# Optimization experiments

Hardware: AMD Instinct MI355X
Metric: run time of the kernel (lower is better)

## Reference

```python
import jax, jax.numpy as jnp
import numpy as np

NUM_HEADS = 4


def lin_interp(f, out_len):
    """Matches torch F.interpolate(mode='linear', align_corners=False) on (B, L_in, D)."""
    L_in = f.shape[1]
    if L_in == out_len:
        return f
    scale = L_in / out_len
    src = (jnp.arange(out_len, dtype=f.dtype) + 0.5) * scale - 0.5
    src = jnp.clip(src, 0.0, L_in - 1)
    i0 = jnp.floor(src).astype(jnp.int32)
    i1 = jnp.minimum(i0 + 1, L_in - 1)
    w = (src - i0.astype(f.dtype))[None, :, None]
    return f[:, i0, :] * (1.0 - w) + f[:, i1, :] * w


def setup_inputs() -> dict:
    key = jax.random.key(0)
    ks = jax.random.split(key, 12)
    D = 256
    s = 1.0 / np.sqrt(D)
    return {
        "branch0": jax.random.normal(ks[0], (8, 4096, D), dtype=jnp.float32),
        "branch1": jax.random.normal(ks[1], (8, 2048, D), dtype=jnp.float32),
        "branch2": jax.random.normal(ks[2], (8, 1024, D), dtype=jnp.float32),
        "Wq": jax.random.normal(ks[3], (D, D), dtype=jnp.float32) * s,
        "bq": jax.random.normal(ks[4], (D,), dtype=jnp.float32) * s,
        "Wk": jax.random.normal(ks[5], (D, D), dtype=jnp.float32) * s,
        "bk": jax.random.normal(ks[6], (D,), dtype=jnp.float32) * s,
        "Wv": jax.random.normal(ks[7], (D, D), dtype=jnp.float32) * s,
        "bv": jax.random.normal(ks[8], (D,), dtype=jnp.float32) * s,
        "Wo": jax.random.normal(ks[9], (D, D), dtype=jnp.float32) * s,
        "bo": jax.random.normal(ks[10], (D,), dtype=jnp.float32) * s,
    }


def reference(branch0, branch1, branch2, Wq, bq, Wk, bk, Wv, bv, Wo, bo):
    branches = [branch0, branch1, branch2]
    max_len = max(f.shape[1] for f in branches)
    # Align all branches to max_len via linear interpolation, stack over branch axis
    x = jnp.stack([lin_interp(f, max_len) for f in branches], axis=1)  # (B, NB, L, D)
    B, NB, L, D = x.shape
    H = NUM_HEADS
    hd = D // H

    def proj(W, b):
        return (x @ W + b).reshape(B, NB, L, H, hd)

    q = proj(Wq, bq)  # (B, NB, L, H, hd)
    k = proj(Wk, bk)
    v = proj(Wv, bv)

    # Attention over branch axis (NB x NB) independently per (head, position)
    attn = jnp.einsum("bnlhd,bmlhd->bhlnm", q, k) / np.sqrt(hd)
    attn = jax.nn.softmax(attn, axis=-1)  # dropout is identity in eval mode
    out = jnp.einsum("bhlnm,bmlhd->bnlhd", attn, v).reshape(B, NB, L, D)
    out = out @ Wo + bo  # (B, NB, L, D)

    # Resize each branch back to its original length
    return tuple(lin_interp(out[:, i], f.shape[1]) for i, f in enumerate(branches))
```

## Files before the change

### kernel.cpp

```cpp
#include <hip/hip_runtime.h>

typedef __attribute__((ext_vector_type(4))) float f32x4;
typedef __attribute__((ext_vector_type(8))) short s16x8;
typedef __attribute__((ext_vector_type(4))) unsigned short u16x4;

__device__ __forceinline__ unsigned short f2bf(float f) {
    union { float f; unsigned int u; } v; v.f = f;
    unsigned int r = v.u + 0x7fffu + ((v.u >> 16) & 1u);
    return (unsigned short)(r >> 16);
}
__device__ __forceinline__ float bf2f(unsigned short h) {
    union { unsigned int u; float f; } v; v.u = ((unsigned int)h) << 16;
    return v.f;
}
__device__ __forceinline__ unsigned int swz(int row, int col) {
    return (unsigned int)(row * 512 + col * 2) ^ (((unsigned int)row & 7u) << 4);
}

__global__ void prep_w(const float* __restrict__ wq, const float* __restrict__ wk,
                       const float* __restrict__ wv, const float* __restrict__ wo,
                       unsigned short* __restrict__ wt2) {
    int idx = blockIdx.x * 256 + threadIdx.x;
    int lane = idx & 63;
    int kt   = (idx >> 6) & 7;
    int nt   = (idx >> 9) & 15;
    int m    = idx >> 13;
    const float* W = (m == 0) ? wq : (m == 1) ? wk : (m == 2) ? wv : wo;
    int g = lane & 15, uu = lane >> 4;
    int n = nt * 16 + g;
    unsigned short* dst = wt2 + (size_t)idx * 8;
    #pragma unroll
    for (int e = 0; e < 8; ++e) {
        int k = kt * 32 + uu * 8 + e;
        dst[e] = f2bf(W[k * 256 + n]);
    }
}

__global__ __launch_bounds__(256, 2)
void fused_attn(const float* __restrict__ br0, const float* __restrict__ br1,
                const float* __restrict__ br2, const unsigned short* __restrict__ wt2,
                const float* __restrict__ bq, const float* __restrict__ bk,
                const float* __restrict__ bv, const float* __restrict__ bo,
                float* __restrict__ out) {
    __shared__ char ldsb[24576];
    char* Xs = ldsb;
    char* Ys = ldsb;

    const int t    = threadIdx.x;
    const int wave = t >> 6;
    const int lane = t & 63;
    const int g    = lane & 15;
    const int u    = lane >> 4;
    const int b    = blockIdx.x >> 8;
    const int l0   = (blockIdx.x & 255) << 4;
    const int nb   = wave * 64;
    const int cc   = lane * 4;

    const s16x8* WF = (const s16x8*)wt2;

    {
        #pragma unroll
        for (int it = 0; it < 12; ++it) {
            int r = it * 4 + wave;
            int n = r >> 4, p = r & 15;
            int l = l0 + p;
            float4 v;
            if (n == 0) {
                v = *(const float4*)(br0 + (size_t)(b * 4096 + l) * 256 + cc);
            } else {
                const float* src = (n == 1) ? br1 : br2;
                int   Lin   = (n == 1) ? 2048 : 1024;
                float scale = (n == 1) ? 0.5f : 0.25f;
                float sp = (l + 0.5f) * scale - 0.5f;
                sp = fminf(fmaxf(sp, 0.0f), (float)(Lin - 1));
                int i0 = (int)sp;
                int i1 = min(i0 + 1, Lin - 1);
                float w = sp - (float)i0;
                float4 a0 = *(const float4*)(src + (size_t)(b * Lin + i0) * 256 + cc);
                float4 a1 = *(const float4*)(src + (size_t)(b * Lin + i1) * 256 + cc);
                v.x = a0.x * (1.0f - w) + a1.x * w;
                v.y = a0.y * (1.0f - w) + a1.y * w;
                v.z = a0.z * (1.0f - w) + a1.z * w;
                v.w = a0.w * (1.0f - w) + a1.w * w;
            }
            u16x4 h;
            h.x = f2bf(v.x); h.y = f2bf(v.y); h.z = f2bf(v.z); h.w = f2bf(v.w);
            *(u16x4*)(Xs + swz(r, cc)) = h;
        }
    }
    __syncthreads();

    float sc[3][3][4];
    {
        f32x4 qc[4][3], kc[4][3];
        #pragma unroll
        for (int tc = 0; tc < 4; ++tc)
            #pragma unroll
            for (int n = 0; n < 3; ++n) {
                qc[tc][n] = (f32x4){0.f, 0.f, 0.f, 0.f};
                kc[tc][n] = (f32x4){0.f, 0.f, 0.f, 0.f};
            }

        __builtin_amdgcn_s_setprio(1);
        #pragma unroll
        for (int kt = 0; kt < 8; ++kt) {
            s16x8 a[3];
            #pragma unroll
            for (int n = 0; n < 3; ++n)
                a[n] = *(const s16x8*)(Xs + swz(n * 16 + g, kt * 32 + u * 8));
            s16x8 bfq[4], bfk[4];
            #pragma unroll
            for (int tc = 0; tc < 4; ++tc) {
                const int ct = wave * 4 + tc;
                bfq[tc] = WF[((0 * 16 + ct) * 8 + kt) * 64 + lane];
                bfk[tc] = WF[((1 * 16 + ct) * 8 + kt) * 64 + lane];
            }
            #pragma unroll
            for (int tc = 0; tc < 4; ++tc)
                #pragma unroll
                for (int n = 0; n < 3; ++n) {
                    qc[tc][n] = __builtin_amdgcn_mfma_f32_16x16x32_bf16(a[n], bfq[tc], qc[tc][n], 0, 0, 0);
                    kc[tc][n] = __builtin_amdgcn_mfma_f32_16x16x32_bf16(a[n], bfk[tc], kc[tc][n], 0, 0, 0);
                }
        }
        __builtin_amdgcn_s_setprio(0);

        #pragma unroll
        for (int n = 0; n < 3; ++n)
            #pragma unroll
            for (int m = 0; m < 3; ++m)
                #pragma unroll
                for (int j = 0; j < 4; ++j) sc[n][m][j] = 0.f;
        #pragma unroll
        for (int tc = 0; tc < 4; ++tc) {
            const float Bqv = bq[nb + tc * 16 + g];
            const float Bkv = bk[nb + tc * 16 + g];
            #pragma unroll
            for (int n = 0; n < 3; ++n)
                #pragma unroll
                for (int j = 0; j < 4; ++j) {
                    qc[tc][n][j] += Bqv;
                    kc[tc][n][j] += Bkv;
                }
            #pragma unroll
            for (int n = 0; n < 3; ++n)
                #pragma unroll
                for (int m = 0; m < 3; ++m)
                    #pragma unroll
                    for (int j = 0; j < 4; ++j)
                        sc[n][m][j] += qc[tc][n][j] * kc[tc][m][j];
        }
        #pragma unroll
        for (int mask = 1; mask < 16; mask <<= 1)
            #pragma unroll
            for (int n = 0; n < 3; ++n)
                #pragma unroll
                for (int m = 0; m < 3; ++m)
                    #pragma unroll
                    for (int j = 0; j < 4; ++j)
                        sc[n][m][j] += __shfl_xor(sc[n][m][j], mask, 16);
        #pragma unroll
        for (int n = 0; n < 3; ++n)
            #pragma unroll
            for (int j = 0; j < 4; ++j) {
                float s0 = sc[n][0][j] * 0.125f;
                float s1 = sc[n][1][j] * 0.125f;
                float s2 = sc[n][2][j] * 0.125f;
                float mx = fmaxf(s0, fmaxf(s1, s2));
                float e0 = __expf(s0 - mx), e1 = __expf(s1 - mx), e2 = __expf(s2 - mx);
                float inv = 1.0f / (e0 + e1 + e2);
                sc[n][0][j] = e0 * inv;
                sc[n][1][j] = e1 * inv;
                sc[n][2][j] = e2 * inv;
            }
    }

    f32x4 vacc[3][4];
    #pragma unroll
    for (int n = 0; n < 3; ++n)
        #pragma unroll
        for (int tc = 0; tc < 4; ++tc)
            vacc[n][tc] = (f32x4){0.f, 0.f, 0.f, 0.f};
    __builtin_amdgcn_s_setprio(1);
    #pragma unroll
    for (int kt = 0; kt < 8; ++kt) {
        s16x8 a[3];
        #pragma unroll
        for (int n = 0; n < 3; ++n)
            a[n] = *(const s16x8*)(Xs + swz(n * 16 + g, kt * 32 + u * 8));
        s16x8 bfv[4];
        #pragma unroll
        for (int tc = 0; tc < 4; ++tc)
            bfv[tc] = WF[((2 * 16 + wave * 4 + tc) * 8 + kt) * 64 + lane];
        #pragma unroll
        for (int tc = 0; tc < 4; ++tc)
            #pragma unroll
            for (int n = 0; n < 3; ++n)
                vacc[n][tc] = __builtin_amdgcn_mfma_f32_16x16x32_bf16(a[n], bfv[tc], vacc[n][tc], 0, 0, 0);
    }
    __builtin_amdgcn_s_setprio(0);
    #pragma unroll
    for (int tc = 0; tc < 4; ++tc) {
        const float Bvv = bv[nb + tc * 16 + g];
        #pragma unroll
        for (int n = 0; n < 3; ++n)
            #pragma unroll
            for (int j = 0; j < 4; ++j)
                vacc[n][tc][j] += Bvv;
    }
    __syncthreads();

    #pragma unroll
    for (int n = 0; n < 3; ++n)
        #pragma unroll
        for (int tc = 0; tc < 4; ++tc)
            #pragma unroll
            for (int j = 0; j < 4; ++j) {
                float o = sc[n][0][j] * vacc[0][tc][j] +
                          sc[n][1][j] * vacc[1][tc][j] +
                          sc[n][2][j] * vacc[2][tc][j];
                *(unsigned short*)(Xs + swz(n * 16 + u * 4 + j, nb + tc * 16 + g)) = f2bf(o);
            }
    __syncthreads();

    f32x4 yacc[3][4];
    #pragma unroll
    for (int n = 0; n < 3; ++n)
        #pragma unroll
        for (int tc = 0; tc < 4; ++tc)
            yacc[n][tc] = (f32x4){0.f, 0.f, 0.f, 0.f};
    __builtin_amdgcn_s_setprio(1);
    #pragma unroll
    for (int kt = 0; kt < 8; ++kt) {
        s16x8 a[3];
        #pragma unroll
        for (int n = 0; n < 3; ++n)
            a[n] = *(const s16x8*)(Xs + swz(n * 16 + g, kt * 32 + u * 8));
        s16x8 bfo[4];
        #pragma unroll
        for (int tc = 0; tc < 4; ++tc)
            bfo[tc] = WF[((3 * 16 + wave * 4 + tc) * 8 + kt) * 64 + lane];
        #pragma unroll
        for (int tc = 0; tc < 4; ++tc)
            #pragma unroll
            for (int n = 0; n < 3; ++n)
                yacc[n][tc] = __builtin_amdgcn_mfma_f32_16x16x32_bf16(a[n], bfo[tc], yacc[n][tc], 0, 0, 0);
    }
    __builtin_amdgcn_s_setprio(0);
    __syncthreads();

    #pragma unroll
    for (int tc = 0; tc < 4; ++tc) {
        int col = nb + tc * 16 + g;
        const float Bov = bo[col];
        #pragma unroll
        for (int j = 0; j < 4; ++j)
            *(unsigned short*)(Ys + swz(u * 4 + j, col)) = f2bf(yacc[0][tc][j] + Bov);
        #pragma unroll
        for (int jj = 0; jj < 2; ++jj)
            *(unsigned short*)(Ys + swz(16 + u * 2 + jj, col)) =
                f2bf(0.5f * (yacc[1][tc][2 * jj] + yacc[1][tc][2 * jj + 1]) + Bov);
        *(unsigned short*)(Ys + swz(24 + u, col)) =
            f2bf(0.5f * (yacc[2][tc][1] + yacc[2][tc][2]) + Bov);
    }
    __syncthreads();

    #pragma unroll
    for (int it = 0; it < 7; ++it) {
        int r = it * 4 + wave;
        u16x4 hv = *(const u16x4*)(Ys + swz(r, cc));
        f32x4 v;
        v.x = bf2f(hv.x); v.y = bf2f(hv.y); v.z = bf2f(hv.z); v.w = bf2f(hv.w);
        float* dst;
        if (r < 16)      dst = out + (size_t)(b * 4096 + l0 + r) * 256 + cc;
        else if (r < 24) dst = out + 8388608 + (size_t)(b * 2048 + (l0 >> 1) + (r - 16)) * 256 + cc;
        else             dst = out + 12582912 + (size_t)(b * 1024 + (l0 >> 2) + (r - 24)) * 256 + cc;
        *(f32x4*)dst = v;
    }
}

extern "C" void kernel_launch(void* const* d_in, const int* in_sizes, int n_in,
                              void* d_out, int out_size, void* d_ws, size_t ws_size,
                              hipStream_t stream) {
    const float* br0 = (const float*)d_in[0];
    const float* br1 = (const float*)d_in[1];
    const float* br2 = (const float*)d_in[2];
    const float* Wq  = (const float*)d_in[3];
    const float* bq  = (const float*)d_in[4];
    const float* Wk  = (const float*)d_in[5];
    const float* bk  = (const float*)d_in[6];
    const float* Wv  = (const float*)d_in[7];
    const float* bv  = (const float*)d_in[8];
    const float* Wo  = (const float*)d_in[9];
    const float* bo  = (const float*)d_in[10];

    unsigned short* wt2 = (unsigned short*)d_ws;

    prep_w<<<128, 256, 0, stream>>>(Wq, Wk, Wv, Wo, wt2);
    fused_attn<<<2048, 256, 0, stream>>>(br0, br1, br2, wt2, bq, bk, bv, bo,
                                         (float*)d_out);
}
```

Baseline: 115.6 us.

## Process 32 positions per block with 8 waves splitting rows into halves

Each block now covers 32 sequence positions instead of 16, using 512 threads where waves 0-3 and 4-7 handle separate 16-row halves over the same column slices. The LDS tile doubles to 48 KB and the grid halves to 1024 blocks. The aim is to amortize block launch and synchronisation overhead and to let the two wave groups share the L2/L1 traffic for weight fragments. In exchange each block needs more LDS and registers, which may lower the number of resident blocks per CU, and there are fewer blocks overall to balance across CUs.

```diff
diff --git a/kernel.cpp b/kernel.cpp
--- a/kernel.cpp
+++ b/kernel.cpp
@@ -36,33 +36,36 @@
     }
 }
 
-__global__ __launch_bounds__(256, 2)
+__global__ __launch_bounds__(512, 2)
 void fused_attn(const float* __restrict__ br0, const float* __restrict__ br1,
                 const float* __restrict__ br2, const unsigned short* __restrict__ wt2,
                 const float* __restrict__ bq, const float* __restrict__ bk,
                 const float* __restrict__ bv, const float* __restrict__ bo,
                 float* __restrict__ out) {
-    __shared__ char ldsb[24576];
+    __shared__ char ldsb[49152];
     char* Xs = ldsb;
     char* Ys = ldsb;
 
     const int t    = threadIdx.x;
     const int wave = t >> 6;
+    const int h    = wave & 3;
+    const int half = wave >> 2;
     const int lane = t & 63;
     const int g    = lane & 15;
     const int u    = lane >> 4;
-    const int b    = blockIdx.x >> 8;
-    const int l0   = (blockIdx.x & 255) << 4;
-    const int nb   = wave * 64;
+    const int b    = blockIdx.x >> 7;
+    const int l0   = (blockIdx.x & 127) << 5;
+    const int nb   = h * 64;
     const int cc   = lane * 4;
+    const int rbase = half * 16;
 
     const s16x8* WF = (const s16x8*)wt2;
 
     {
         #pragma unroll
         for (int it = 0; it < 12; ++it) {
-            int r = it * 4 + wave;
-            int n = r >> 4, p = r & 15;
+            int r = it * 8 + wave;
+            int n = r >> 5, p = r & 31;
             int l = l0 + p;
             float4 v;
             if (n == 0) {
@@ -83,9 +86,9 @@
                 v.z = a0.z * (1.0f - w) + a1.z * w;
                 v.w = a0.w * (1.0f - w) + a1.w * w;
             }
-            u16x4 h;
-            h.x = f2bf(v.x); h.y = f2bf(v.y); h.z = f2bf(v.z); h.w = f2bf(v.w);
-            *(u16x4*)(Xs + swz(r, cc)) = h;
+            u16x4 hv;
+            hv.x = f2bf(v.x); hv.y = f2bf(v.y); hv.z = f2bf(v.z); hv.w = f2bf(v.w);
+            *(u16x4*)(Xs + swz(r, cc)) = hv;
         }
     }
     __syncthreads();
@@ -107,11 +110,11 @@
             s16x8 a[3];
             #pragma unroll
             for (int n = 0; n < 3; ++n)
-                a[n] = *(const s16x8*)(Xs + swz(n * 16 + g, kt * 32 + u * 8));
+                a[n] = *(const s16x8*)(Xs + swz(n * 32 + rbase + g, kt * 32 + u * 8));
             s16x8 bfq[4], bfk[4];
             #pragma unroll
             for (int tc = 0; tc < 4; ++tc) {
-                const int ct = wave * 4 + tc;
+                const int ct = h * 4 + tc;
                 bfq[tc] = WF[((0 * 16 + ct) * 8 + kt) * 64 + lane];
                 bfk[tc] = WF[((1 * 16 + ct) * 8 + kt) * 64 + lane];
             }
@@ -187,11 +190,11 @@
         s16x8 a[3];
         #pragma unroll
         for (int n = 0; n < 3; ++n)
-            a[n] = *(const s16x8*)(Xs + swz(n * 16 + g, kt * 32 + u * 8));
+            a[n] = *(const s16x8*)(Xs + swz(n * 32 + rbase + g, kt * 32 + u * 8));
         s16x8 bfv[4];
         #pragma unroll
         for (int tc = 0; tc < 4; ++tc)
-            bfv[tc] = WF[((2 * 16 + wave * 4 + tc) * 8 + kt) * 64 + lane];
+            bfv[tc] = WF[((2 * 16 + h * 4 + tc) * 8 + kt) * 64 + lane];
         #pragma unroll
         for (int tc = 0; tc < 4; ++tc)
             #pragma unroll
@@ -219,7 +222,8 @@
                 float o = sc[n][0][j] * vacc[0][tc][j] +
                           sc[n][1][j] * vacc[1][tc][j] +
                           sc[n][2][j] * vacc[2][tc][j];
-                *(unsigned short*)(Xs + swz(n * 16 + u * 4 + j, nb + tc * 16 + g)) = f2bf(o);
+                int row = n * 32 + rbase + u * 4 + j;
+                *(unsigned short*)(Xs + swz(row, nb + tc * 16 + g)) = f2bf(o);
             }
     __syncthreads();
 
@@ -235,11 +239,11 @@
         s16x8 a[3];
         #pragma unroll
         for (int n = 0; n < 3; ++n)
-            a[n] = *(const s16x8*)(Xs + swz(n * 16 + g, kt * 32 + u * 8));
+            a[n] = *(const s16x8*)(Xs + swz(n * 32 + rbase + g, kt * 32 + u * 8));
         s16x8 bfo[4];
         #pragma unroll
         for (int tc = 0; tc < 4; ++tc)
-            bfo[tc] = WF[((3 * 16 + wave * 4 + tc) * 8 + kt) * 64 + lane];
+            bfo[tc] = WF[((3 * 16 + h * 4 + tc) * 8 + kt) * 64 + lane];
         #pragma unroll
         for (int tc = 0; tc < 4; ++tc)
             #pragma unroll
@@ -255,26 +259,27 @@
         const float Bov = bo[col];
         #pragma unroll
         for (int j = 0; j < 4; ++j)
-            *(unsigned short*)(Ys + swz(u * 4 + j, col)) = f2bf(yacc[0][tc][j] + Bov);
+            *(unsigned short*)(Ys + swz(rbase + u * 4 + j, col)) =
+                f2bf(yacc[0][tc][j] + Bov);
         #pragma unroll
         for (int jj = 0; jj < 2; ++jj)
-            *(unsigned short*)(Ys + swz(16 + u * 2 + jj, col)) =
+            *(unsigned short*)(Ys + swz(32 + half * 8 + u * 2 + jj, col)) =
                 f2bf(0.5f * (yacc[1][tc][2 * jj] + yacc[1][tc][2 * jj + 1]) + Bov);
-        *(unsigned short*)(Ys + swz(24 + u, col)) =
+        *(unsigned short*)(Ys + swz(48 + half * 4 + u, col)) =
             f2bf(0.5f * (yacc[2][tc][1] + yacc[2][tc][2]) + Bov);
     }
     __syncthreads();
 
     #pragma unroll
     for (int it = 0; it < 7; ++it) {
-        int r = it * 4 + wave;
+        int r = it * 8 + wave;
         u16x4 hv = *(const u16x4*)(Ys + swz(r, cc));
         f32x4 v;
         v.x = bf2f(hv.x); v.y = bf2f(hv.y); v.z = bf2f(hv.z); v.w = bf2f(hv.w);
         float* dst;
-        if (r < 16)      dst = out + (size_t)(b * 4096 + l0 + r) * 256 + cc;
-        else if (r < 24) dst = out + 8388608 + (size_t)(b * 2048 + (l0 >> 1) + (r - 16)) * 256 + cc;
-        else             dst = out + 12582912 + (size_t)(b * 1024 + (l0 >> 2) + (r - 24)) * 256 + cc;
+        if (r < 32)      dst = out + (size_t)(b * 4096 + l0 + r) * 256 + cc;
+        else if (r < 48) dst = out + 8388608 + (size_t)(b * 2048 + (l0 >> 1) + (r - 32)) * 256 + cc;
+        else             dst = out + 12582912 + (size_t)(b * 1024 + (l0 >> 2) + (r - 48)) * 256 + cc;
         *(f32x4*)dst = v;
     }
 }
@@ -297,6 +302,6 @@
     unsigned short* wt2 = (unsigned short*)d_ws;
 
     prep_w<<<128, 256, 0, stream>>>(Wq, Wk, Wv, Wo, wt2);
-    fused_attn<<<2048, 256, 0, stream>>>(br0, br1, br2, wt2, bq, bk, bv, bo,
+    fused_attn<<<1024, 512, 0, stream>>>(br0, br1, br2, wt2, bq, bk, bv, bo,
                                          (float*)d_out);
 }
```

After: 117.5 us. About the same (+1.7%).
